# Optimization experiments

Measured on AMD Instinct MI355X. Metric: run time of the kernel, lower is better.

## Reference

```python
import jax, jax.numpy as jnp
import numpy as np

F, H, K, T, IT, S = 128, 128, 768, 4, 2, 57  # feat, hidden, max_child, edge types, iters, num_sem


def setup_inputs() -> dict:
    key = jax.random.key(0)
    ks = jax.random.split(key, 12)

    def w(k, shape):
        fan = shape[0] if len(shape) == 2 else shape[1]
        return jax.random.normal(k, shape, jnp.float32) * fan ** -0.5

    return {
        "parent_feature": jax.random.normal(ks[0], (1, F), jnp.float32),
        "W_parent": w(ks[1], (F, H * K)), "b_parent": jnp.zeros((H * K,), jnp.float32),
        "W_exists": w(ks[2], (H, 1)), "b_exists": jnp.zeros((1,), jnp.float32),
        "W_edge_lat": w(ks[3], (2 * H, H)), "b_edge_lat": jnp.zeros((H,), jnp.float32),
        "W_edge_ex": w(ks[4], (T, H)), "b_edge_ex": jnp.zeros((T,), jnp.float32),
        "W_ne": w(ks[5], (IT, 2 * H, H)), "b_ne": jnp.zeros((IT, H), jnp.float32),
        "W_child": w(ks[6], (H * (IT + 1), H)), "b_child": jnp.zeros((H,), jnp.float32),
        "W_sem": w(ks[7], (H, S)), "b_sem": jnp.zeros((S,), jnp.float32),
        "W_child2": w(ks[8], (H, F)), "b_child2": jnp.zeros((F,), jnp.float32),
    }


def reference(parent_feature, W_parent, b_parent, W_exists, b_exists,
              W_edge_lat, b_edge_lat, W_edge_ex, b_edge_ex,
              W_ne, b_ne, W_child, b_child, W_sem, b_sem, W_child2, b_child2):
    # parent -> K child latents
    x = jax.nn.relu(parent_feature @ W_parent + b_parent)  # [1, K*H]
    cf = x.reshape(1, K, H)                                 # child feats
    exists_logits = cf @ W_exists + b_exists                # [1, K, 1]

    # pairwise edge latents [1, K, K, 2H] -> [1, K, K, H]
    pair0 = jnp.concatenate([
        jnp.broadcast_to(cf[:, :, None, :], (1, K, K, H)),
        jnp.broadcast_to(cf[:, None, :, :], (1, K, K, H))], axis=3)
    elat = jax.nn.relu(pair0 @ W_edge_lat + b_edge_lat)
    edge_logits = jnp.einsum('bijh,th->bijt', elat, W_edge_ex) + b_edge_ex  # [1,K,K,T]

    # fixed edge set: existing edges between existing nodes (dense mask form)
    exists = exists_logits[0, :, 0] > 0                     # [K]
    emask = jnp.any(edge_logits[0] > 0, axis=-1) & exists[:, None] & exists[None, :]
    any_edge = jnp.any(emask)

    feats = [cf]
    for i in range(IT):
        c = cf[0]                                           # [K, H]
        pair = jnp.concatenate([
            jnp.broadcast_to(c[:, None, :], (K, K, H)),
            jnp.broadcast_to(c[None, :, :], (K, K, H))], axis=2)
        msg = jax.nn.relu(pair @ W_ne[i] + b_ne[i])         # [K, K, H], >= 0
        msg = jnp.where(emask[:, :, None], msg, 0.0)
        # scatter_max with zeros-initialized out == max over masked neighbors (msg >= 0)
        new_cf = msg.max(axis=1)[None]                      # [1, K, H]
        cf = jnp.where(any_edge, new_cf, cf)                # no edges -> feats unchanged
        feats.append(cf)

    h = jnp.concatenate(feats, axis=2).reshape(K, H * (IT + 1))
    h = jax.nn.relu(h @ W_child + b_child)                  # [K, H]
    sem_logits = (h @ W_sem + b_sem).reshape(1, K, S)
    child_out = jax.nn.relu(h @ W_child2 + b_child2).reshape(1, K, F)
    return child_out, sem_logits, exists_logits, edge_logits
```

## Files before the change

kernel.cpp:

```cpp
#include <hip/hip_runtime.h>
#include <hip/hip_bf16.h>


#define NK 768
#define NH 128
#define NCF 98304

__global__ __launch_bounds__(256) void k_parent(const float* __restrict__ pf,
    const float* __restrict__ Wp, const float* __restrict__ bp,
    const float* __restrict__ Wexi, const float* __restrict__ bexi,
    float* __restrict__ cf0, float* __restrict__ exO, unsigned int* __restrict__ flag)
{
    __shared__ float s_pf[128];
    __shared__ float4 s_part[8][32];
    int t = threadIdx.x;
    if (t < 128) s_pf[t] = pf[t];
    if (blockIdx.x == 0 && t == 0) *flag = 0u;
    __syncthreads();
    int c = t & 31, g = t >> 5;
    int col4 = blockIdx.x * 32 + c;
    const float4* W4 = (const float4*)Wp;
    float4 acc = make_float4(0.f, 0.f, 0.f, 0.f);
    #pragma unroll
    for (int q = 0; q < 16; ++q) {
        int f = g * 16 + q;
        float4 w = W4[(size_t)f * 24576 + col4];
        float p = s_pf[f];
        acc.x = fmaf(p, w.x, acc.x);
        acc.y = fmaf(p, w.y, acc.y);
        acc.z = fmaf(p, w.z, acc.z);
        acc.w = fmaf(p, w.w, acc.w);
    }
    s_part[g][c] = acc;
    __syncthreads();
    if (t < 32) {
        float4 r = s_part[0][t];
        #pragma unroll
        for (int q = 1; q < 8; ++q) {
            float4 p = s_part[q][t];
            r.x += p.x; r.y += p.y; r.z += p.z; r.w += p.w;
        }
        float4 bi = ((const float4*)bp)[col4];
        r.x = fmaxf(r.x + bi.x, 0.f);
        r.y = fmaxf(r.y + bi.y, 0.f);
        r.z = fmaxf(r.z + bi.z, 0.f);
        r.w = fmaxf(r.w + bi.w, 0.f);
        ((float4*)cf0)[col4] = r;
        float4 w = ((const float4*)Wexi)[t];
        float dot = r.x * w.x + r.y * w.y + r.z * w.z + r.w * w.w;
        dot += __shfl_xor(dot, 16);
        dot += __shfl_xor(dot, 8);
        dot += __shfl_xor(dot, 4);
        dot += __shfl_xor(dot, 2);
        dot += __shfl_xor(dot, 1);
        if (t == 0) exO[blockIdx.x] = dot + bexi[0];
    }
}

__global__ __launch_bounds__(512) void k_dualmm(const float* __restrict__ src,
    const float* __restrict__ Wel, float* __restrict__ A, float* __restrict__ BT,
    const float* __restrict__ Wne, float* __restrict__ A0, float* __restrict__ B0)
{
    __shared__ float s_cf[4][128];
    __shared__ float s_bt[128][4];
    int t = threadIdx.x;
    int k0 = blockIdx.x * 4;
    int set = blockIdx.y;
    s_cf[t >> 7][t & 127] = src[k0 * 128 + t];
    __syncthreads();
    int h = t & 127, sub = (t >> 7) & 1, half = t >> 8;
    const float* W = (set ? Wne : Wel) + half * 16384;
    const float* c0 = &s_cf[sub * 2][0];
    const float* c1 = &s_cf[sub * 2 + 1][0];
    float a0 = 0.f, a1 = 0.f;
    #pragma unroll 8
    for (int r = 0; r < 128; ++r) {
        float w = W[r * 128 + h];
        a0 = fmaf(c0[r], w, a0);
        a1 = fmaf(c1[r], w, a1);
    }
    if (half == 0) {
        float* D = set ? A0 : A;
        D[(k0 + sub * 2) * 128 + h] = a0;
        D[(k0 + sub * 2 + 1) * 128 + h] = a1;
    } else if (set) {
        B0[(k0 + sub * 2) * 128 + h] = a0;
        B0[(k0 + sub * 2 + 1) * 128 + h] = a1;
    } else {
        s_bt[h][sub * 2] = a0;
        s_bt[h][sub * 2 + 1] = a1;
    }
    __syncthreads();
    if (set == 0 && t < 128)
        *(float4*)(BT + (size_t)t * NK + k0) = *(const float4*)&s_bt[t][0];
}

__global__ __launch_bounds__(256) void k_edge(const float* __restrict__ A,
    const float* __restrict__ BT, const float* __restrict__ b_lat,
    const float* __restrict__ Wex, const float* __restrict__ bex,
    const float* __restrict__ exO, float* __restrict__ edge_out,
    unsigned char* __restrict__ mask, unsigned int* __restrict__ flag)
{
    __shared__ float4 s_A[128];
    __shared__ float4 s_W[128];
    __shared__ float s_B[2][16][256];
    __shared__ float s_exi[4];
    __shared__ unsigned int s_any;
    int t = threadIdx.x;
    int i0 = blockIdx.x * 4;
    int j0 = blockIdx.y * 256;
    int j = j0 + t;
    if (t < 128) {
        float bl = b_lat[t];
        s_A[t] = make_float4(A[(i0 + 0) * 128 + t] + bl, A[(i0 + 1) * 128 + t] + bl,
                             A[(i0 + 2) * 128 + t] + bl, A[(i0 + 3) * 128 + t] + bl);
        s_W[t] = make_float4(Wex[t], Wex[128 + t], Wex[256 + t], Wex[384 + t]);
    }
    if (t < 4) s_exi[t] = exO[i0 + t];
    if (t == 0) s_any = 0u;
    const float4* BT4 = (const float4*)BT;
    int row = t >> 6, col = t & 63;
    {
        #pragma unroll
        for (int k = 0; k < 4; ++k)
            *(float4*)&s_B[0][row + k * 4][col * 4] =
                BT4[(size_t)(row + k * 4) * 192 + blockIdx.y * 64 + col];
    }
    __syncthreads();
    float4 l0 = make_float4(0.f,0.f,0.f,0.f), l1 = l0, l2 = l0, l3 = l0;
    for (int c = 0; c < 8; ++c) {
        float4 r0, r1, r2, r3;
        if (c < 7) {
            size_t base = (size_t)((c + 1) * 16 + row) * 192 + blockIdx.y * 64 + col;
            r0 = BT4[base];
            r1 = BT4[base + 4 * 192];
            r2 = BT4[base + 8 * 192];
            r3 = BT4[base + 12 * 192];
        }
        int buf = c & 1;
        #pragma unroll
        for (int hh = 0; hh < 16; ++hh) {
            float bv = s_B[buf][hh][t];
            float4 av = s_A[c * 16 + hh];
            float4 wv = s_W[c * 16 + hh];
            float e0 = fmaxf(av.x + bv, 0.f);
            float e1 = fmaxf(av.y + bv, 0.f);
            float e2 = fmaxf(av.z + bv, 0.f);
            float e3 = fmaxf(av.w + bv, 0.f);
            l0.x = fmaf(e0, wv.x, l0.x); l0.y = fmaf(e0, wv.y, l0.y);
            l0.z = fmaf(e0, wv.z, l0.z); l0.w = fmaf(e0, wv.w, l0.w);
            l1.x = fmaf(e1, wv.x, l1.x); l1.y = fmaf(e1, wv.y, l1.y);
            l1.z = fmaf(e1, wv.z, l1.z); l1.w = fmaf(e1, wv.w, l1.w);
            l2.x = fmaf(e2, wv.x, l2.x); l2.y = fmaf(e2, wv.y, l2.y);
            l2.z = fmaf(e2, wv.z, l2.z); l2.w = fmaf(e2, wv.w, l2.w);
            l3.x = fmaf(e3, wv.x, l3.x); l3.y = fmaf(e3, wv.y, l3.y);
            l3.z = fmaf(e3, wv.z, l3.z); l3.w = fmaf(e3, wv.w, l3.w);
        }
        if (c < 7) {
            int nb = (c + 1) & 1;
            *(float4*)&s_B[nb][row + 0][col * 4] = r0;
            *(float4*)&s_B[nb][row + 4][col * 4] = r1;
            *(float4*)&s_B[nb][row + 8][col * 4] = r2;
            *(float4*)&s_B[nb][row + 12][col * 4] = r3;
        }
        __syncthreads();
    }
    float b0 = bex[0], b1 = bex[1], b2 = bex[2], b3 = bex[3];
    bool ej = exO[j] > 0.f;
    float4 v0 = make_float4(l0.x + b0, l0.y + b1, l0.z + b2, l0.w + b3);
    float4 v1 = make_float4(l1.x + b0, l1.y + b1, l1.z + b2, l1.w + b3);
    float4 v2 = make_float4(l2.x + b0, l2.y + b1, l2.z + b2, l2.w + b3);
    float4 v3 = make_float4(l3.x + b0, l3.y + b1, l3.z + b2, l3.w + b3);
    ((float4*)edge_out)[(size_t)(i0 + 0) * NK + j] = v0;
    ((float4*)edge_out)[(size_t)(i0 + 1) * NK + j] = v1;
    ((float4*)edge_out)[(size_t)(i0 + 2) * NK + j] = v2;
    ((float4*)edge_out)[(size_t)(i0 + 3) * NK + j] = v3;
    bool m0 = ((v0.x > 0.f) | (v0.y > 0.f) | (v0.z > 0.f) | (v0.w > 0.f)) && ej && (s_exi[0] > 0.f);
    bool m1 = ((v1.x > 0.f) | (v1.y > 0.f) | (v1.z > 0.f) | (v1.w > 0.f)) && ej && (s_exi[1] > 0.f);
    bool m2 = ((v2.x > 0.f) | (v2.y > 0.f) | (v2.z > 0.f) | (v2.w > 0.f)) && ej && (s_exi[2] > 0.f);
    bool m3 = ((v3.x > 0.f) | (v3.y > 0.f) | (v3.z > 0.f) | (v3.w > 0.f)) && ej && (s_exi[3] > 0.f);
    mask[(i0 + 0) * NK + j] = m0 ? (unsigned char)1 : (unsigned char)0;
    mask[(i0 + 1) * NK + j] = m1 ? (unsigned char)1 : (unsigned char)0;
    mask[(i0 + 2) * NK + j] = m2 ? (unsigned char)1 : (unsigned char)0;
    mask[(i0 + 3) * NK + j] = m3 ? (unsigned char)1 : (unsigned char)0;
    unsigned long long bal = __ballot((m0 | m1 | m2 | m3) ? 1 : 0);
    if ((t & 63) == 0 && bal) s_any = 1u;
    __syncthreads();
    if (t == 0 && s_any) *flag = 1u;
}

__global__ __launch_bounds__(256) void k_msgmax(const float* __restrict__ Bm,
    const unsigned char* __restrict__ mask, float* __restrict__ Mp)
{
    __shared__ float s_madd[192][4];
    __shared__ float s_red[4][256];
    int t = threadIdx.x;
    int h = t & 127, s = t >> 7;
    int i0 = blockIdx.x * 4;
    int j0 = blockIdx.y * 192;
    for (int idx = t; idx < 768; idx += 256) {
        int i = idx / 192, jj = idx - i * 192;
        s_madd[jj][i] = mask[(i0 + i) * NK + j0 + jj] ? 0.f : -1e30f;
    }
    __syncthreads();
    float M0 = -1e30f, M1 = -1e30f, M2 = -1e30f, M3 = -1e30f;
    const float* bp2 = Bm + (size_t)(j0 + s * 96) * 128 + h;
    #pragma unroll 8
    for (int jj = 0; jj < 96; ++jj) {
        float bv = bp2[(size_t)jj * 128];
        float4 m = *(const float4*)&s_madd[s * 96 + jj][0];
        M0 = fmaxf(M0, bv + m.x);
        M1 = fmaxf(M1, bv + m.y);
        M2 = fmaxf(M2, bv + m.z);
        M3 = fmaxf(M3, bv + m.w);
    }
    s_red[0][t] = M0; s_red[1][t] = M1; s_red[2][t] = M2; s_red[3][t] = M3;
    __syncthreads();
    if (s == 0) {
        Mp[(size_t)blockIdx.y * NCF + (i0 + 0) * 128 + h] = fmaxf(M0, s_red[0][128 + h]);
        Mp[(size_t)blockIdx.y * NCF + (i0 + 1) * 128 + h] = fmaxf(M1, s_red[1][128 + h]);
        Mp[(size_t)blockIdx.y * NCF + (i0 + 2) * 128 + h] = fmaxf(M2, s_red[2][128 + h]);
        Mp[(size_t)blockIdx.y * NCF + (i0 + 3) * 128 + h] = fmaxf(M3, s_red[3][128 + h]);
    }
}

__global__ __launch_bounds__(512) void k_dualmm_c(const float* __restrict__ Mp,
    const float* __restrict__ A0, const float* __restrict__ bne,
    const float* __restrict__ cf0, const unsigned int* __restrict__ flag,
    float* __restrict__ cf1, const float* __restrict__ Wne1,
    float* __restrict__ A1, float* __restrict__ B1)
{
    __shared__ float s_cf[2][128];
    int t = threadIdx.x;
    int k0 = blockIdx.x * 2;
    unsigned int fl = *flag;
    if (t < 256) {
        int kk = t >> 7, hh = t & 127;
        int g = (k0 + kk) * 128 + hh;
        float M = fmaxf(fmaxf(Mp[g], Mp[NCF + g]), fmaxf(Mp[2 * NCF + g], Mp[3 * NCF + g]));
        float v = fl ? fmaxf(A0[g] + bne[hh] + M, 0.f) : cf0[g];
        s_cf[kk][hh] = v;
        cf1[g] = v;
    }
    __syncthreads();
    int h = t & 127, kk = (t >> 7) & 1, half = t >> 8;
    const float* W = Wne1 + half * 16384;
    const float* c = &s_cf[kk][0];
    float acc = 0.f;
    #pragma unroll 8
    for (int r = 0; r < 128; ++r)
        acc = fmaf(c[r], W[r * 128 + h], acc);
    float* D = half ? B1 : A1;
    D[(k0 + kk) * 128 + h] = acc;
}

__global__ __launch_bounds__(512) void k_final(const float* __restrict__ cf0,
    const float* __restrict__ cf1, const float* __restrict__ Mp,
    const float* __restrict__ A1, const float* __restrict__ bne1,
    const unsigned int* __restrict__ flag,
    const float* __restrict__ Wc, const float* __restrict__ bc,
    const float* __restrict__ Wsem, const float* __restrict__ bsem,
    const float* __restrict__ W2, const float* __restrict__ b2,
    float* __restrict__ out)
{
    __shared__ float s_f[2][384];
    __shared__ float s_h[2][128];
    __shared__ float s_hp[2][128];
    int t = threadIdx.x;
    int k0 = blockIdx.x * 2;
    unsigned int fl = *flag;
    for (int idx = t; idx < 768; idx += 512) {
        int kk = idx >= 384 ? 1 : 0;
        int c = idx - kk * 384;
        int row = k0 + kk;
        float v;
        if (c < 128) v = cf0[row * 128 + c];
        else if (c < 256) v = cf1[row * 128 + (c - 128)];
        else {
            int hh = c - 256, g = row * 128 + hh;
            float M = fmaxf(fmaxf(Mp[g], Mp[NCF + g]), fmaxf(Mp[2 * NCF + g], Mp[3 * NCF + g]));
            v = fl ? fmaxf(A1[g] + bne1[hh] + M, 0.f) : cf1[g];
        }
        s_f[kk][c] = v;
    }
    __syncthreads();
    int h = t & 127, rh = (t >> 7) & 1, kg = t >> 8;
    float acc = 0.f;
    {
        const float* f = &s_f[kg][rh * 192];
        const float* Wcp = Wc + rh * 192 * 128;
        #pragma unroll 8
        for (int r = 0; r < 192; ++r)
            acc = fmaf(f[r], Wcp[r * 128 + h], acc);
    }
    if (rh) s_hp[kg][h] = acc;
    __syncthreads();
    if (!rh) s_h[kg][h] = fmaxf(acc + s_hp[kg][h] + bc[h], 0.f);
    __syncthreads();
    float a2 = 0.f;
    {
        const float* hr = &s_h[kg][rh * 64];
        const float* W2p = W2 + rh * 64 * 128;
        #pragma unroll 8
        for (int r = 0; r < 64; ++r)
            a2 = fmaf(hr[r], W2p[r * 128 + h], a2);
    }
    if (rh) s_hp[kg][h] = a2;
    __syncthreads();
    if (!rh) out[(size_t)(k0 + kg) * 128 + h] = fmaxf(a2 + s_hp[kg][h] + b2[h], 0.f);
    if (t < 114) {
        int kk = t / 57, sidx = t - kk * 57;
        float ss = bsem[sidx];
        const float* hr = &s_h[kk][0];
        #pragma unroll 8
        for (int r = 0; r < 128; ++r)
            ss = fmaf(hr[r], Wsem[r * 57 + sidx], ss);
        out[98304 + (size_t)(k0 + kk) * 57 + sidx] = ss;
    }
}

extern "C" void kernel_launch(void* const* d_in, const int* in_sizes, int n_in,
                              void* d_out, int out_size, void* d_ws, size_t ws_size,
                              hipStream_t stream) {
    const float* pf   = (const float*)d_in[0];
    const float* Wp   = (const float*)d_in[1];
    const float* bp   = (const float*)d_in[2];
    const float* Wexi = (const float*)d_in[3];
    const float* bexi = (const float*)d_in[4];
    const float* Wel  = (const float*)d_in[5];
    const float* bel  = (const float*)d_in[6];
    const float* Wee  = (const float*)d_in[7];
    const float* bee  = (const float*)d_in[8];
    const float* Wne  = (const float*)d_in[9];
    const float* bne  = (const float*)d_in[10];
    const float* Wc   = (const float*)d_in[11];
    const float* bc   = (const float*)d_in[12];
    const float* Wsem = (const float*)d_in[13];
    const float* bsem = (const float*)d_in[14];
    const float* W2   = (const float*)d_in[15];
    const float* b2   = (const float*)d_in[16];
    float* out = (float*)d_out;
    float* ws  = (float*)d_ws;
    const int N = NCF;
    float* cf0 = ws;
    float* cf1 = ws + N;
    float* A   = ws + 2 * N;
    float* BT  = ws + 3 * N;
    float* A0  = ws + 4 * N;
    float* B0  = ws + 5 * N;
    float* A1  = ws + 6 * N;
    float* B1  = ws + 7 * N;
    float* Mp  = ws + 8 * N;
    unsigned char* mask = (unsigned char*)(ws + 12 * N);
    unsigned int* flag  = (unsigned int*)(mask + 589824);

    float* out_ex   = out + 142080;
    float* out_edge = out + 142848;

    k_parent<<<768, 256, 0, stream>>>(pf, Wp, bp, Wexi, bexi, cf0, out_ex, flag);
    k_dualmm<<<dim3(192, 2), 512, 0, stream>>>(cf0, Wel, A, BT, Wne, A0, B0);
    k_edge<<<dim3(192, 3), 256, 0, stream>>>(A, BT, bel, Wee, bee, out_ex, out_edge, mask, flag);
    k_msgmax<<<dim3(192, 4), 256, 0, stream>>>(B0, mask, Mp);
    k_dualmm_c<<<384, 512, 0, stream>>>(Mp, A0, bne, cf0, flag, cf1, Wne + 32768, A1, B1);
    k_msgmax<<<dim3(192, 4), 256, 0, stream>>>(B1, mask, Mp);
    k_final<<<384, 512, 0, stream>>>(cf0, cf1, Mp, A1, bne + 128, flag,
                                     Wc, bc, Wsem, bsem, W2, b2, out);
}
```

Baseline: 83.57 us.

## Fuse masked message max with downstream matmuls and pack edge FMAs as float2

Merges each masked max-reduction over neighbors into the kernel that consumes it, so each block handles two rows over all 768 neighbors instead of writing four partial maxima to a workspace buffer and re-reading them. This cuts the launch count from seven to five and removes the partial-max buffer traffic. The edge kernel's accumulators are repacked into two-wide vectors so the compiler can emit packed FP32 FMA/max instructions, and the exists load is hoisted to the start. The trade-off is less parallelism per reduction: 384 blocks each stream all of B through a longer serial loop, and the final matmuls run on half as many threads per block.

```diff
diff --git a/kernel.cpp b/kernel.cpp
--- a/kernel.cpp
+++ b/kernel.cpp
@@ -5,6 +5,8 @@
 #define NK 768
 #define NH 128
 #define NCF 98304
+
+typedef float v2f __attribute__((ext_vector_type(2)));
 
 __global__ __launch_bounds__(256) void k_parent(const float* __restrict__ pf,
     const float* __restrict__ Wp, const float* __restrict__ bp,
@@ -108,8 +110,8 @@
     __shared__ unsigned int s_any;
     int t = threadIdx.x;
     int i0 = blockIdx.x * 4;
-    int j0 = blockIdx.y * 256;
-    int j = j0 + t;
+    int j = blockIdx.y * 256 + t;
+    float exj = exO[j];
     if (t < 128) {
         float bl = b_lat[t];
         s_A[t] = make_float4(A[(i0 + 0) * 128 + t] + bl, A[(i0 + 1) * 128 + t] + bl,
@@ -127,7 +129,7 @@
                 BT4[(size_t)(row + k * 4) * 192 + blockIdx.y * 64 + col];
     }
     __syncthreads();
-    float4 l0 = make_float4(0.f,0.f,0.f,0.f), l1 = l0, l2 = l0, l3 = l0;
+    v2f l01[4] = {}, l23[4] = {};
     for (int c = 0; c < 8; ++c) {
         float4 r0, r1, r2, r3;
         if (c < 7) {
@@ -143,18 +145,12 @@
             float bv = s_B[buf][hh][t];
             float4 av = s_A[c * 16 + hh];
             float4 wv = s_W[c * 16 + hh];
-            float e0 = fmaxf(av.x + bv, 0.f);
-            float e1 = fmaxf(av.y + bv, 0.f);
-            float e2 = fmaxf(av.z + bv, 0.f);
-            float e3 = fmaxf(av.w + bv, 0.f);
-            l0.x = fmaf(e0, wv.x, l0.x); l0.y = fmaf(e0, wv.y, l0.y);
-            l0.z = fmaf(e0, wv.z, l0.z); l0.w = fmaf(e0, wv.w, l0.w);
-            l1.x = fmaf(e1, wv.x, l1.x); l1.y = fmaf(e1, wv.y, l1.y);
-            l1.z = fmaf(e1, wv.z, l1.z); l1.w = fmaf(e1, wv.w, l1.w);
-            l2.x = fmaf(e2, wv.x, l2.x); l2.y = fmaf(e2, wv.y, l2.y);
-            l2.z = fmaf(e2, wv.z, l2.z); l2.w = fmaf(e2, wv.w, l2.w);
-            l3.x = fmaf(e3, wv.x, l3.x); l3.y = fmaf(e3, wv.y, l3.y);
-            l3.z = fmaf(e3, wv.z, l3.z); l3.w = fmaf(e3, wv.w, l3.w);
+            v2f e01 = __builtin_elementwise_max((v2f){av.x + bv, av.y + bv}, (v2f){0.f, 0.f});
+            v2f e23 = __builtin_elementwise_max((v2f){av.z + bv, av.w + bv}, (v2f){0.f, 0.f});
+            l01[0] += e01 * wv.x; l01[1] += e01 * wv.y;
+            l01[2] += e01 * wv.z; l01[3] += e01 * wv.w;
+            l23[0] += e23 * wv.x; l23[1] += e23 * wv.y;
+            l23[2] += e23 * wv.z; l23[3] += e23 * wv.w;
         }
         if (c < 7) {
             int nb = (c + 1) & 1;
@@ -166,11 +162,11 @@
         __syncthreads();
     }
     float b0 = bex[0], b1 = bex[1], b2 = bex[2], b3 = bex[3];
-    bool ej = exO[j] > 0.f;
-    float4 v0 = make_float4(l0.x + b0, l0.y + b1, l0.z + b2, l0.w + b3);
-    float4 v1 = make_float4(l1.x + b0, l1.y + b1, l1.z + b2, l1.w + b3);
-    float4 v2 = make_float4(l2.x + b0, l2.y + b1, l2.z + b2, l2.w + b3);
-    float4 v3 = make_float4(l3.x + b0, l3.y + b1, l3.z + b2, l3.w + b3);
+    bool ej = exj > 0.f;
+    float4 v0 = make_float4(l01[0].x + b0, l01[1].x + b1, l01[2].x + b2, l01[3].x + b3);
+    float4 v1 = make_float4(l01[0].y + b0, l01[1].y + b1, l01[2].y + b2, l01[3].y + b3);
+    float4 v2 = make_float4(l23[0].x + b0, l23[1].x + b1, l23[2].x + b2, l23[3].x + b3);
+    float4 v3 = make_float4(l23[0].y + b0, l23[1].y + b1, l23[2].y + b2, l23[3].y + b3);
     ((float4*)edge_out)[(size_t)(i0 + 0) * NK + j] = v0;
     ((float4*)edge_out)[(size_t)(i0 + 1) * NK + j] = v1;
     ((float4*)edge_out)[(size_t)(i0 + 2) * NK + j] = v2;
@@ -189,125 +185,129 @@
     if (t == 0 && s_any) *flag = 1u;
 }
 
-__global__ __launch_bounds__(256) void k_msgmax(const float* __restrict__ Bm,
-    const unsigned char* __restrict__ mask, float* __restrict__ Mp)
-{
-    __shared__ float s_madd[192][4];
-    __shared__ float s_red[4][256];
-    int t = threadIdx.x;
+__global__ __launch_bounds__(256) void k_msg1(const float* __restrict__ B0m,
+    const unsigned char* __restrict__ mask, const float* __restrict__ A0,
+    const float* __restrict__ bne, const float* __restrict__ cf0,
+    const unsigned int* __restrict__ flag, float* __restrict__ cf1,
+    const float* __restrict__ Wne1, float* __restrict__ A1, float* __restrict__ B1)
+{
+    __shared__ float s_madd[768][2];
+    __shared__ float s_red[2][256];
+    __shared__ float s_cf[2][128];
+    int t = threadIdx.x;
+    int i0 = blockIdx.x * 2;
+    for (int idx = t; idx < 1536; idx += 256) {
+        int i = idx & 1, jj = idx >> 1;
+        s_madd[jj][i] = mask[(i0 + i) * NK + jj] ? 0.f : -1e30f;
+    }
+    __syncthreads();
     int h = t & 127, s = t >> 7;
-    int i0 = blockIdx.x * 4;
-    int j0 = blockIdx.y * 192;
-    for (int idx = t; idx < 768; idx += 256) {
-        int i = idx / 192, jj = idx - i * 192;
-        s_madd[jj][i] = mask[(i0 + i) * NK + j0 + jj] ? 0.f : -1e30f;
-    }
-    __syncthreads();
-    float M0 = -1e30f, M1 = -1e30f, M2 = -1e30f, M3 = -1e30f;
-    const float* bp2 = Bm + (size_t)(j0 + s * 96) * 128 + h;
+    float M0 = -1e30f, M1 = -1e30f;
+    const float* bp2 = B0m + (size_t)(s * 384) * 128 + h;
     #pragma unroll 8
-    for (int jj = 0; jj < 96; ++jj) {
+    for (int jj = 0; jj < 384; ++jj) {
         float bv = bp2[(size_t)jj * 128];
-        float4 m = *(const float4*)&s_madd[s * 96 + jj][0];
+        float2 m = *(const float2*)&s_madd[s * 384 + jj][0];
         M0 = fmaxf(M0, bv + m.x);
         M1 = fmaxf(M1, bv + m.y);
-        M2 = fmaxf(M2, bv + m.z);
-        M3 = fmaxf(M3, bv + m.w);
-    }
-    s_red[0][t] = M0; s_red[1][t] = M1; s_red[2][t] = M2; s_red[3][t] = M3;
-    __syncthreads();
+    }
+    s_red[0][t] = M0;
+    s_red[1][t] = M1;
+    __syncthreads();
+    unsigned int fl = *flag;
     if (s == 0) {
-        Mp[(size_t)blockIdx.y * NCF + (i0 + 0) * 128 + h] = fmaxf(M0, s_red[0][128 + h]);
-        Mp[(size_t)blockIdx.y * NCF + (i0 + 1) * 128 + h] = fmaxf(M1, s_red[1][128 + h]);
-        Mp[(size_t)blockIdx.y * NCF + (i0 + 2) * 128 + h] = fmaxf(M2, s_red[2][128 + h]);
-        Mp[(size_t)blockIdx.y * NCF + (i0 + 3) * 128 + h] = fmaxf(M3, s_red[3][128 + h]);
-    }
-}
-
-__global__ __launch_bounds__(512) void k_dualmm_c(const float* __restrict__ Mp,
-    const float* __restrict__ A0, const float* __restrict__ bne,
-    const float* __restrict__ cf0, const unsigned int* __restrict__ flag,
-    float* __restrict__ cf1, const float* __restrict__ Wne1,
-    float* __restrict__ A1, float* __restrict__ B1)
-{
-    __shared__ float s_cf[2][128];
-    int t = threadIdx.x;
-    int k0 = blockIdx.x * 2;
-    unsigned int fl = *flag;
-    if (t < 256) {
-        int kk = t >> 7, hh = t & 127;
-        int g = (k0 + kk) * 128 + hh;
-        float M = fmaxf(fmaxf(Mp[g], Mp[NCF + g]), fmaxf(Mp[2 * NCF + g], Mp[3 * NCF + g]));
-        float v = fl ? fmaxf(A0[g] + bne[hh] + M, 0.f) : cf0[g];
-        s_cf[kk][hh] = v;
-        cf1[g] = v;
-    }
-    __syncthreads();
-    int h = t & 127, kk = (t >> 7) & 1, half = t >> 8;
-    const float* W = Wne1 + half * 16384;
-    const float* c = &s_cf[kk][0];
-    float acc = 0.f;
+        M0 = fmaxf(M0, s_red[0][128 + h]);
+        M1 = fmaxf(M1, s_red[1][128 + h]);
+        int g0 = i0 * 128 + h, g1 = (i0 + 1) * 128 + h;
+        float bh = bne[h];
+        float v0 = fl ? fmaxf(A0[g0] + bh + M0, 0.f) : cf0[g0];
+        float v1 = fl ? fmaxf(A0[g1] + bh + M1, 0.f) : cf0[g1];
+        s_cf[0][h] = v0; s_cf[1][h] = v1;
+        cf1[g0] = v0; cf1[g1] = v1;
+    }
+    __syncthreads();
+    const float* W = Wne1 + s * 16384;
+    const float* c0 = &s_cf[0][0];
+    const float* c1 = &s_cf[1][0];
+    float a0 = 0.f, a1 = 0.f;
     #pragma unroll 8
-    for (int r = 0; r < 128; ++r)
-        acc = fmaf(c[r], W[r * 128 + h], acc);
-    float* D = half ? B1 : A1;
-    D[(k0 + kk) * 128 + h] = acc;
-}
-
-__global__ __launch_bounds__(512) void k_final(const float* __restrict__ cf0,
-    const float* __restrict__ cf1, const float* __restrict__ Mp,
-    const float* __restrict__ A1, const float* __restrict__ bne1,
-    const unsigned int* __restrict__ flag,
+    for (int r = 0; r < 128; ++r) {
+        float w = W[r * 128 + h];
+        a0 = fmaf(c0[r], w, a0);
+        a1 = fmaf(c1[r], w, a1);
+    }
+    float* D = s ? B1 : A1;
+    D[i0 * 128 + h] = a0;
+    D[(i0 + 1) * 128 + h] = a1;
+}
+
+__global__ __launch_bounds__(256) void k_msg2(const float* __restrict__ B1m,
+    const unsigned char* __restrict__ mask, const float* __restrict__ A1,
+    const float* __restrict__ bne1, const float* __restrict__ cf0,
+    const float* __restrict__ cf1, const unsigned int* __restrict__ flag,
     const float* __restrict__ Wc, const float* __restrict__ bc,
     const float* __restrict__ Wsem, const float* __restrict__ bsem,
     const float* __restrict__ W2, const float* __restrict__ b2,
     float* __restrict__ out)
 {
+    __shared__ float s_madd[768][2];
+    __shared__ float s_red[2][256];
     __shared__ float s_f[2][384];
     __shared__ float s_h[2][128];
-    __shared__ float s_hp[2][128];
-    int t = threadIdx.x;
-    int k0 = blockIdx.x * 2;
+    int t = threadIdx.x;
+    int i0 = blockIdx.x * 2;
+    for (int idx = t; idx < 1536; idx += 256) {
+        int i = idx & 1, jj = idx >> 1;
+        s_madd[jj][i] = mask[(i0 + i) * NK + jj] ? 0.f : -1e30f;
+    }
+    __syncthreads();
+    int h = t & 127, s = t >> 7;
+    float M0 = -1e30f, M1 = -1e30f;
+    const float* bp2 = B1m + (size_t)(s * 384) * 128 + h;
+    #pragma unroll 8
+    for (int jj = 0; jj < 384; ++jj) {
+        float bv = bp2[(size_t)jj * 128];
+        float2 m = *(const float2*)&s_madd[s * 384 + jj][0];
+        M0 = fmaxf(M0, bv + m.x);
+        M1 = fmaxf(M1, bv + m.y);
+    }
+    s_red[0][t] = M0;
+    s_red[1][t] = M1;
+    __syncthreads();
     unsigned int fl = *flag;
-    for (int idx = t; idx < 768; idx += 512) {
-        int kk = idx >= 384 ? 1 : 0;
-        int c = idx - kk * 384;
-        int row = k0 + kk;
-        float v;
-        if (c < 128) v = cf0[row * 128 + c];
-        else if (c < 256) v = cf1[row * 128 + (c - 128)];
-        else {
-            int hh = c - 256, g = row * 128 + hh;
-            float M = fmaxf(fmaxf(Mp[g], Mp[NCF + g]), fmaxf(Mp[2 * NCF + g], Mp[3 * NCF + g]));
-            v = fl ? fmaxf(A1[g] + bne1[hh] + M, 0.f) : cf1[g];
-        }
-        s_f[kk][c] = v;
-    }
-    __syncthreads();
-    int h = t & 127, rh = (t >> 7) & 1, kg = t >> 8;
+    int g0 = i0 * 128 + h, g1 = (i0 + 1) * 128 + h;
+    if (s == 0) {
+        M0 = fmaxf(M0, s_red[0][128 + h]);
+        M1 = fmaxf(M1, s_red[1][128 + h]);
+        float bh = bne1[h];
+        float f10 = cf1[g0], f11 = cf1[g1];
+        s_f[0][256 + h] = fl ? fmaxf(A1[g0] + bh + M0, 0.f) : f10;
+        s_f[1][256 + h] = fl ? fmaxf(A1[g1] + bh + M1, 0.f) : f11;
+        s_f[0][128 + h] = f10;
+        s_f[1][128 + h] = f11;
+    } else {
+        s_f[0][h] = cf0[g0];
+        s_f[1][h] = cf0[g1];
+    }
+    __syncthreads();
+    int kg = s;
     float acc = 0.f;
     {
-        const float* f = &s_f[kg][rh * 192];
-        const float* Wcp = Wc + rh * 192 * 128;
+        const float* f = &s_f[kg][0];
         #pragma unroll 8
-        for (int r = 0; r < 192; ++r)
-            acc = fmaf(f[r], Wcp[r * 128 + h], acc);
-    }
-    if (rh) s_hp[kg][h] = acc;
-    __syncthreads();
-    if (!rh) s_h[kg][h] = fmaxf(acc + s_hp[kg][h] + bc[h], 0.f);
+        for (int r = 0; r < 384; ++r)
+            acc = fmaf(f[r], Wc[r * 128 + h], acc);
+    }
+    s_h[kg][h] = fmaxf(acc + bc[h], 0.f);
     __syncthreads();
     float a2 = 0.f;
     {
-        const float* hr = &s_h[kg][rh * 64];
-        const float* W2p = W2 + rh * 64 * 128;
+        const float* hr = &s_h[kg][0];
         #pragma unroll 8
-        for (int r = 0; r < 64; ++r)
-            a2 = fmaf(hr[r], W2p[r * 128 + h], a2);
-    }
-    if (rh) s_hp[kg][h] = a2;
-    __syncthreads();
-    if (!rh) out[(size_t)(k0 + kg) * 128 + h] = fmaxf(a2 + s_hp[kg][h] + b2[h], 0.f);
+        for (int r = 0; r < 128; ++r)
+            a2 = fmaf(hr[r], W2[r * 128 + h], a2);
+    }
+    out[(size_t)(i0 + kg) * 128 + h] = fmaxf(a2 + b2[h], 0.f);
     if (t < 114) {
         int kk = t / 57, sidx = t - kk * 57;
         float ss = bsem[sidx];
@@ -315,7 +315,7 @@
         #pragma unroll 8
         for (int r = 0; r < 128; ++r)
             ss = fmaf(hr[r], Wsem[r * 57 + sidx], ss);
-        out[98304 + (size_t)(k0 + kk) * 57 + sidx] = ss;
+        out[98304 + (size_t)(i0 + kk) * 57 + sidx] = ss;
     }
 }
 
@@ -350,8 +350,7 @@
     float* B0  = ws + 5 * N;
     float* A1  = ws + 6 * N;
     float* B1  = ws + 7 * N;
-    float* Mp  = ws + 8 * N;
-    unsigned char* mask = (unsigned char*)(ws + 12 * N);
+    unsigned char* mask = (unsigned char*)(ws + 8 * N);
     unsigned int* flag  = (unsigned int*)(mask + 589824);
 
     float* out_ex   = out + 142080;
@@ -360,9 +359,7 @@
     k_parent<<<768, 256, 0, stream>>>(pf, Wp, bp, Wexi, bexi, cf0, out_ex, flag);
     k_dualmm<<<dim3(192, 2), 512, 0, stream>>>(cf0, Wel, A, BT, Wne, A0, B0);
     k_edge<<<dim3(192, 3), 256, 0, stream>>>(A, BT, bel, Wee, bee, out_ex, out_edge, mask, flag);
-    k_msgmax<<<dim3(192, 4), 256, 0, stream>>>(B0, mask, Mp);
-    k_dualmm_c<<<384, 512, 0, stream>>>(Mp, A0, bne, cf0, flag, cf1, Wne + 32768, A1, B1);
-    k_msgmax<<<dim3(192, 4), 256, 0, stream>>>(B1, mask, Mp);
-    k_final<<<384, 512, 0, stream>>>(cf0, cf1, Mp, A1, bne + 128, flag,
-                                     Wc, bc, Wsem, bsem, W2, b2, out);
-}
+    k_msg1<<<384, 256, 0, stream>>>(B0, mask, A0, bne, cf0, flag, cf1, Wne + 32768, A1, B1);
+    k_msg2<<<384, 256, 0, stream>>>(B1, mask, A1, bne + 128, cf0, cf1, flag,
+                                    Wc, bc, Wsem, bsem, W2, b2, out);
+}
```

Result: slower. 103.6 us (+24.0%).

## Retile masked message-max with shared B tiles and packed float2 math

Applied to the files above, without the earlier changes.

Rewrites the masked max-reduction kernel so each block handles 8 rows by 96 neighbors. Neighbor features are staged through shared memory in 32-row tiles, and each thread reduces two packed columns for two rows. The j-split grows from 4 to 8 partials, so the combine steps now max over 8 slices and the workspace offset for the mask moves. The edge kernel's inner FMA loop is recast to two-wide vector types so the compiler can emit packed FP32 ops, and the exists load is hoisted ahead of the main loop. In exchange, more partial results are written and re-read in the combine kernels.

```diff
diff --git a/kernel.cpp b/kernel.cpp
--- a/kernel.cpp
+++ b/kernel.cpp
@@ -5,6 +5,8 @@
 #define NK 768
 #define NH 128
 #define NCF 98304
+
+typedef float v2f __attribute__((ext_vector_type(2)));
 
 __global__ __launch_bounds__(256) void k_parent(const float* __restrict__ pf,
     const float* __restrict__ Wp, const float* __restrict__ bp,
@@ -108,8 +110,8 @@
     __shared__ unsigned int s_any;
     int t = threadIdx.x;
     int i0 = blockIdx.x * 4;
-    int j0 = blockIdx.y * 256;
-    int j = j0 + t;
+    int j = blockIdx.y * 256 + t;
+    float exj = exO[j];
     if (t < 128) {
         float bl = b_lat[t];
         s_A[t] = make_float4(A[(i0 + 0) * 128 + t] + bl, A[(i0 + 1) * 128 + t] + bl,
@@ -127,7 +129,7 @@
                 BT4[(size_t)(row + k * 4) * 192 + blockIdx.y * 64 + col];
     }
     __syncthreads();
-    float4 l0 = make_float4(0.f,0.f,0.f,0.f), l1 = l0, l2 = l0, l3 = l0;
+    v2f l01[4] = {}, l23[4] = {};
     for (int c = 0; c < 8; ++c) {
         float4 r0, r1, r2, r3;
         if (c < 7) {
@@ -143,18 +145,12 @@
             float bv = s_B[buf][hh][t];
             float4 av = s_A[c * 16 + hh];
             float4 wv = s_W[c * 16 + hh];
-            float e0 = fmaxf(av.x + bv, 0.f);
-            float e1 = fmaxf(av.y + bv, 0.f);
-            float e2 = fmaxf(av.z + bv, 0.f);
-            float e3 = fmaxf(av.w + bv, 0.f);
-            l0.x = fmaf(e0, wv.x, l0.x); l0.y = fmaf(e0, wv.y, l0.y);
-            l0.z = fmaf(e0, wv.z, l0.z); l0.w = fmaf(e0, wv.w, l0.w);
-            l1.x = fmaf(e1, wv.x, l1.x); l1.y = fmaf(e1, wv.y, l1.y);
-            l1.z = fmaf(e1, wv.z, l1.z); l1.w = fmaf(e1, wv.w, l1.w);
-            l2.x = fmaf(e2, wv.x, l2.x); l2.y = fmaf(e2, wv.y, l2.y);
-            l2.z = fmaf(e2, wv.z, l2.z); l2.w = fmaf(e2, wv.w, l2.w);
-            l3.x = fmaf(e3, wv.x, l3.x); l3.y = fmaf(e3, wv.y, l3.y);
-            l3.z = fmaf(e3, wv.z, l3.z); l3.w = fmaf(e3, wv.w, l3.w);
+            v2f e01 = __builtin_elementwise_max((v2f){av.x + bv, av.y + bv}, (v2f){0.f, 0.f});
+            v2f e23 = __builtin_elementwise_max((v2f){av.z + bv, av.w + bv}, (v2f){0.f, 0.f});
+            l01[0] += e01 * wv.x; l01[1] += e01 * wv.y;
+            l01[2] += e01 * wv.z; l01[3] += e01 * wv.w;
+            l23[0] += e23 * wv.x; l23[1] += e23 * wv.y;
+            l23[2] += e23 * wv.z; l23[3] += e23 * wv.w;
         }
         if (c < 7) {
             int nb = (c + 1) & 1;
@@ -166,11 +162,11 @@
         __syncthreads();
     }
     float b0 = bex[0], b1 = bex[1], b2 = bex[2], b3 = bex[3];
-    bool ej = exO[j] > 0.f;
-    float4 v0 = make_float4(l0.x + b0, l0.y + b1, l0.z + b2, l0.w + b3);
-    float4 v1 = make_float4(l1.x + b0, l1.y + b1, l1.z + b2, l1.w + b3);
-    float4 v2 = make_float4(l2.x + b0, l2.y + b1, l2.z + b2, l2.w + b3);
-    float4 v3 = make_float4(l3.x + b0, l3.y + b1, l3.z + b2, l3.w + b3);
+    bool ej = exj > 0.f;
+    float4 v0 = make_float4(l01[0].x + b0, l01[1].x + b1, l01[2].x + b2, l01[3].x + b3);
+    float4 v1 = make_float4(l01[0].y + b0, l01[1].y + b1, l01[2].y + b2, l01[3].y + b3);
+    float4 v2 = make_float4(l23[0].x + b0, l23[1].x + b1, l23[2].x + b2, l23[3].x + b3);
+    float4 v3 = make_float4(l23[0].y + b0, l23[1].y + b1, l23[2].y + b2, l23[3].y + b3);
     ((float4*)edge_out)[(size_t)(i0 + 0) * NK + j] = v0;
     ((float4*)edge_out)[(size_t)(i0 + 1) * NK + j] = v1;
     ((float4*)edge_out)[(size_t)(i0 + 2) * NK + j] = v2;
@@ -189,42 +185,44 @@
     if (t == 0 && s_any) *flag = 1u;
 }
 
-__global__ __launch_bounds__(256) void k_msgmax(const float* __restrict__ Bm,
+__global__ __launch_bounds__(256) void k_mm(const float* __restrict__ Bm,
     const unsigned char* __restrict__ mask, float* __restrict__ Mp)
 {
-    __shared__ float s_madd[192][4];
-    __shared__ float s_red[4][256];
-    int t = threadIdx.x;
-    int h = t & 127, s = t >> 7;
-    int i0 = blockIdx.x * 4;
-    int j0 = blockIdx.y * 192;
+    __shared__ float s_B[32][128];
+    __shared__ float s_madd[96][8];
+    int t = threadIdx.x;
+    int i0 = blockIdx.x * 8;
+    int j0 = blockIdx.y * 96;
     for (int idx = t; idx < 768; idx += 256) {
-        int i = idx / 192, jj = idx - i * 192;
+        int jj = idx >> 3, i = idx & 7;
         s_madd[jj][i] = mask[(i0 + i) * NK + j0 + jj] ? 0.f : -1e30f;
     }
-    __syncthreads();
-    float M0 = -1e30f, M1 = -1e30f, M2 = -1e30f, M3 = -1e30f;
-    const float* bp2 = Bm + (size_t)(j0 + s * 96) * 128 + h;
-    #pragma unroll 8
-    for (int jj = 0; jj < 96; ++jj) {
-        float bv = bp2[(size_t)jj * 128];
-        float4 m = *(const float4*)&s_madd[s * 96 + jj][0];
-        M0 = fmaxf(M0, bv + m.x);
-        M1 = fmaxf(M1, bv + m.y);
-        M2 = fmaxf(M2, bv + m.z);
-        M3 = fmaxf(M3, bv + m.w);
-    }
-    s_red[0][t] = M0; s_red[1][t] = M1; s_red[2][t] = M2; s_red[3][t] = M3;
-    __syncthreads();
-    if (s == 0) {
-        Mp[(size_t)blockIdx.y * NCF + (i0 + 0) * 128 + h] = fmaxf(M0, s_red[0][128 + h]);
-        Mp[(size_t)blockIdx.y * NCF + (i0 + 1) * 128 + h] = fmaxf(M1, s_red[1][128 + h]);
-        Mp[(size_t)blockIdx.y * NCF + (i0 + 2) * 128 + h] = fmaxf(M2, s_red[2][128 + h]);
-        Mp[(size_t)blockIdx.y * NCF + (i0 + 3) * 128 + h] = fmaxf(M3, s_red[3][128 + h]);
-    }
-}
-
-__global__ __launch_bounds__(512) void k_dualmm_c(const float* __restrict__ Mp,
+    int p = t & 63, g = t >> 6;
+    v2f M0 = {-1e30f, -1e30f}, M1 = {-1e30f, -1e30f};
+    const float4* B4 = (const float4*)Bm;
+    for (int c = 0; c < 3; ++c) {
+        __syncthreads();
+        #pragma unroll
+        for (int k = 0; k < 4; ++k) {
+            int idx = t + k * 256;
+            ((float4*)s_B)[idx] = B4[(size_t)(j0 + c * 32) * 32 + idx];
+        }
+        __syncthreads();
+        #pragma unroll 8
+        for (int jj = 0; jj < 32; ++jj) {
+            v2f b = *(const v2f*)&s_B[jj][2 * p];
+            float m0 = s_madd[c * 32 + jj][2 * g];
+            float m1 = s_madd[c * 32 + jj][2 * g + 1];
+            M0 = __builtin_elementwise_max(M0, b + (v2f){m0, m0});
+            M1 = __builtin_elementwise_max(M1, b + (v2f){m1, m1});
+        }
+    }
+    float* Mb = Mp + (size_t)blockIdx.y * NCF;
+    *(v2f*)&Mb[(i0 + 2 * g) * 128 + 2 * p] = M0;
+    *(v2f*)&Mb[(i0 + 2 * g + 1) * 128 + 2 * p] = M1;
+}
+
+__global__ __launch_bounds__(512) void k_cmb1(const float* __restrict__ Mp,
     const float* __restrict__ A0, const float* __restrict__ bne,
     const float* __restrict__ cf0, const unsigned int* __restrict__ flag,
     float* __restrict__ cf1, const float* __restrict__ Wne1,
@@ -237,7 +235,9 @@
     if (t < 256) {
         int kk = t >> 7, hh = t & 127;
         int g = (k0 + kk) * 128 + hh;
-        float M = fmaxf(fmaxf(Mp[g], Mp[NCF + g]), fmaxf(Mp[2 * NCF + g], Mp[3 * NCF + g]));
+        float M = Mp[g];
+        #pragma unroll
+        for (int q = 1; q < 8; ++q) M = fmaxf(M, Mp[q * NCF + g]);
         float v = fl ? fmaxf(A0[g] + bne[hh] + M, 0.f) : cf0[g];
         s_cf[kk][hh] = v;
         cf1[g] = v;
@@ -278,7 +278,9 @@
         else if (c < 256) v = cf1[row * 128 + (c - 128)];
         else {
             int hh = c - 256, g = row * 128 + hh;
-            float M = fmaxf(fmaxf(Mp[g], Mp[NCF + g]), fmaxf(Mp[2 * NCF + g], Mp[3 * NCF + g]));
+            float M = Mp[g];
+            #pragma unroll
+            for (int q = 1; q < 8; ++q) M = fmaxf(M, Mp[q * NCF + g]);
             v = fl ? fmaxf(A1[g] + bne1[hh] + M, 0.f) : cf1[g];
         }
         s_f[kk][c] = v;
@@ -351,7 +353,7 @@
     float* A1  = ws + 6 * N;
     float* B1  = ws + 7 * N;
     float* Mp  = ws + 8 * N;
-    unsigned char* mask = (unsigned char*)(ws + 12 * N);
+    unsigned char* mask = (unsigned char*)(ws + 16 * N);
     unsigned int* flag  = (unsigned int*)(mask + 589824);
 
     float* out_ex   = out + 142080;
@@ -360,9 +362,9 @@
     k_parent<<<768, 256, 0, stream>>>(pf, Wp, bp, Wexi, bexi, cf0, out_ex, flag);
     k_dualmm<<<dim3(192, 2), 512, 0, stream>>>(cf0, Wel, A, BT, Wne, A0, B0);
     k_edge<<<dim3(192, 3), 256, 0, stream>>>(A, BT, bel, Wee, bee, out_ex, out_edge, mask, flag);
-    k_msgmax<<<dim3(192, 4), 256, 0, stream>>>(B0, mask, Mp);
-    k_dualmm_c<<<384, 512, 0, stream>>>(Mp, A0, bne, cf0, flag, cf1, Wne + 32768, A1, B1);
-    k_msgmax<<<dim3(192, 4), 256, 0, stream>>>(B1, mask, Mp);
+    k_mm<<<dim3(96, 8), 256, 0, stream>>>(B0, mask, Mp);
+    k_cmb1<<<384, 512, 0, stream>>>(Mp, A0, bne, cf0, flag, cf1, Wne + 32768, A1, B1);
+    k_mm<<<dim3(96, 8), 256, 0, stream>>>(B1, mask, Mp);
     k_final<<<384, 512, 0, stream>>>(cf0, cf1, Mp, A1, bne + 128, flag,
                                      Wc, bc, Wsem, bsem, W2, b2, out);
 }
```

New measurement: 83.45 us. About the same (-0.2%).
